# Kernel tuning notes

Measured on AMD Instinct MI355X. Metric: run time of the kernel, lower is better.

The kernel has to match this reference:

```python
import jax, jax.numpy as jnp
import numpy as np

LOG2PI = float(np.log(2.0 * np.pi))


def setup_inputs() -> dict:
    key = jax.random.key(0)
    ks = jax.random.split(key, 5)
    B, T, XD, C = 128, 2050, 6, 64
    return {
        "x": jax.random.normal(ks[0], (B, T, XD), jnp.float32),
        "observation_means": jax.random.uniform(ks[1], (C, XD), dtype=jnp.float32),
        "observation_stddevs": jax.random.uniform(ks[2], (C, XD), dtype=jnp.float32),
        "log_A": jax.random.normal(ks[3], (C, C), jnp.float32),
        "log_pi": jax.random.normal(ks[4], (C,), jnp.float32),
    }


def _emission_logprob(x, means, stds):
    # Normal(means[:, :4], relu(stds[:, :4]) + 0.1).log_prob(x[:, :, :4]) summed over feat dim
    mu = means[:, :4]                       # (C,4)
    sigma = jax.nn.relu(stds[:, :4]) + 0.1  # (C,4)
    z = (x[:, :, None, :4] - mu) / sigma    # (B,T,C,4)
    return jnp.sum(-0.5 * z * z - jnp.log(sigma) - 0.5 * LOG2PI, axis=-1)  # (B,T,C)


def _forward_scalers(logp, log_A, log_pi):
    # scaled HMM forward pass; returns per-step log normalizers (T,B)
    a0 = logp[:, 0] + log_pi
    s0 = jax.nn.logsumexp(a0, axis=-1)
    a0n = a0 - s0[:, None]

    def step(a_prev, lp_t):
        a = lp_t + jax.nn.logsumexp(a_prev[:, :, None] + log_A[None], axis=1)
        s = jax.nn.logsumexp(a, axis=-1)
        return a - s[:, None], s

    _, s_rest = jax.lax.scan(step, a0n, jnp.swapaxes(logp[:, 1:], 0, 1))
    return jnp.concatenate([s0[None], s_rest], axis=0)  # (T,B)


def _viterbi(logp, log_A, log_pi):
    d0 = logp[:, 0] + log_pi  # (B,C)

    def step(d_prev, lp_t):
        scores = d_prev[:, :, None] + log_A[None]  # (B,C_prev,C_cur)
        psi_t = jnp.argmax(scores, axis=1)
        d = jnp.max(scores, axis=1) + lp_t
        return d, psi_t

    d_last, psi = jax.lax.scan(step, d0, jnp.swapaxes(logp[:, 1:], 0, 1))  # psi: (T-1,B,C)
    c_last = jnp.argmax(d_last, axis=-1)  # (B,)

    def back(c_next, psi_t):
        c_t = jnp.take_along_axis(psi_t, c_next[:, None], axis=1)[:, 0]
        return c_t, c_t

    _, cs = jax.lax.scan(back, c_last, psi, reverse=True)  # (T-1,B)
    c = jnp.concatenate([cs, c_last[None]], axis=0)  # (T,B)
    return jnp.swapaxes(c, 0, 1)  # (B,T)


def reference(x, observation_means, observation_stddevs, log_A, log_pi):
    logA = jax.nn.log_softmax(log_A, axis=1)
    logpi = jax.nn.log_softmax(log_pi, axis=0)
    logp = _emission_logprob(x, observation_means, observation_stddevs)  # (B,T,C)
    scalers = _forward_scalers(logp, logA, logpi)                         # (T,B)
    logp_x = jnp.sum(scalers, axis=0)                                     # (B,)
    c_est = _viterbi(logp, logA, logpi)                                   # (B,T) int
    return logp_x, c_est
```

## Files before the change

kernel.cpp:

```cpp
#include <hip/hip_runtime.h>

#define T_LEN 2050
#define B_SZ 128
#define NCHUNK 33
#define HL2PI 0.91893853320467274178f

__device__ __forceinline__ float waveMax(float v) {
#pragma unroll
    for (int off = 32; off >= 1; off >>= 1)
        v = fmaxf(v, __shfl_xor(v, off, 64));
    return v;
}
__device__ __forceinline__ float waveSum(float v) {
#pragma unroll
    for (int off = 32; off >= 1; off >>= 1)
        v += __shfl_xor(v, off, 64);
    return v;
}
__device__ __forceinline__ void waveArgmax(float& v, int& idx) {
#pragma unroll
    for (int off = 32; off >= 1; off >>= 1) {
        float ov = __shfl_xor(v, off, 64);
        int   oi = __shfl_xor(idx, off, 64);
        if (ov > v || (ov == v && oi < idx)) { v = ov; idx = oi; }
    }
}
__device__ __forceinline__ void cfence() { asm volatile("" ::: "memory"); }

__device__ __forceinline__ float rl(float v, int lane) {
    return __int_as_float(__builtin_amdgcn_readlane(__float_as_int(v), lane));
}

__device__ __forceinline__ float dppSumAll(float v) {
#define SSTEP(ctrl) { int t_ = __builtin_amdgcn_update_dpp(0, __float_as_int(v), ctrl, 0xf, 0xf, true); \
                      v = v + __int_as_float(t_); }
    SSTEP(0x111) SSTEP(0x112) SSTEP(0x114) SSTEP(0x118) SSTEP(0x142) SSTEP(0x143)
#undef SSTEP
    return __int_as_float(__builtin_amdgcn_readlane(__float_as_int(v), 63));
}
__device__ __forceinline__ float dppMaxAll(float v) {
#define MSTEP(ctrl) { int t_ = __builtin_amdgcn_update_dpp(__float_as_int(v), __float_as_int(v), ctrl, 0xf, 0xf, false); \
                      v = fmaxf(v, __int_as_float(t_)); }
    MSTEP(0x111) MSTEP(0x112) MSTEP(0x114) MSTEP(0x118) MSTEP(0x142) MSTEP(0x143)
#undef MSTEP
    return __int_as_float(__builtin_amdgcn_readlane(__float_as_int(v), 63));
}

extern "C" __global__ __launch_bounds__(64, 1)
void hmm_prep(const float* __restrict__ logA_in,
              const float* __restrict__ logpi_in,
              float* __restrict__ lAg,
              float* __restrict__ lpig)
{
    __shared__ float la[64 * 65];
    __shared__ float rowlse[64];
    const int j = threadIdx.x;
#pragma unroll
    for (int k = 0; k < 64; ++k)
        la[k * 65 + j] = logA_in[k * 64 + j];
    cfence();
    {
        float m = -1e30f;
#pragma unroll
        for (int k = 0; k < 64; ++k) m = fmaxf(m, la[j * 65 + k]);
        float s = 0.f;
#pragma unroll
        for (int k = 0; k < 64; ++k) s += expf(la[j * 65 + k] - m);
        rowlse[j] = m + logf(s);
    }
    cfence();
    {
        float v = logpi_in[j];
        float m = waveMax(v);
        float s = waveSum(expf(v - m));
        lpig[j] = v - (m + logf(s));
    }
    float4* o = (float4*)lAg;
#pragma unroll
    for (int k = 0; k < 16; ++k) {
        float4 v;
        v.x = la[(4 * k + 0) * 65 + j] - rowlse[4 * k + 0];
        v.y = la[(4 * k + 1) * 65 + j] - rowlse[4 * k + 1];
        v.z = la[(4 * k + 2) * 65 + j] - rowlse[4 * k + 2];
        v.w = la[(4 * k + 3) * 65 + j] - rowlse[4 * k + 3];
        o[j * 16 + k] = v;
    }
}

extern "C" __global__ __launch_bounds__(256)
void hmm_emis(const float* __restrict__ x,
              const float* __restrict__ means,
              const float* __restrict__ stds,
              float* __restrict__ buf,
              float* __restrict__ m_pre)
{
    const int wid = blockIdx.x * 4 + (threadIdx.x >> 6);
    const int j = threadIdx.x & 63;
    const int t = wid >> 7;
    const int b = wid & 127;

    const float* xt = x + ((size_t)b * T_LEN + t) * 6;
    float x0 = xt[0], x1 = xt[1], x2 = xt[2], x3 = xt[3];

    float mu0 = means[j * 6 + 0], mu1 = means[j * 6 + 1];
    float mu2 = means[j * 6 + 2], mu3 = means[j * 6 + 3];
    float sg0 = fmaxf(stds[j * 6 + 0], 0.f) + 0.1f;
    float sg1 = fmaxf(stds[j * 6 + 1], 0.f) + 0.1f;
    float sg2 = fmaxf(stds[j * 6 + 2], 0.f) + 0.1f;
    float sg3 = fmaxf(stds[j * 6 + 3], 0.f) + 0.1f;
    float ls0 = logf(sg0), ls1 = logf(sg1), ls2 = logf(sg2), ls3 = logf(sg3);

    float z0 = (x0 - mu0) / sg0, z1 = (x1 - mu1) / sg1;
    float z2 = (x2 - mu2) / sg2, z3 = (x3 - mu3) / sg3;
    float e0 = ((-0.5f * z0) * z0 - ls0) - HL2PI;
    float e1 = ((-0.5f * z1) * z1 - ls1) - HL2PI;
    float e2 = ((-0.5f * z2) * z2 - ls2) - HL2PI;
    float e3 = ((-0.5f * z3) * z3 - ls3) - HL2PI;
    float lp = ((e0 + e1) + e2) + e3;

    buf[((size_t)b * T_LEN + t) * 64 + j] = lp;
    float mm = waveMax(lp);
    if (j == 0) m_pre[(size_t)b * T_LEN + t] = mm;
}

#define FWD_REDUCE(SRC)                                                   \
    float q0 = 0.f, q1 = 0.f, q2 = 0.f, q3 = 0.f;                         \
    _Pragma("unroll")                                                     \
    for (int gq = 0; gq < 4; ++gq) {                                      \
        float s_[16];                                                     \
        _Pragma("unroll")                                                 \
        for (int m_ = 0; m_ < 16; ++m_) s_[m_] = rl((SRC), 16 * gq + m_); \
        __builtin_amdgcn_sched_barrier(0);                                \
        _Pragma("unroll")                                                 \
        for (int k2 = 0; k2 < 4; ++k2) {                                  \
            const int i_ = 16 * gq + 4 * k2;                              \
            q0 = fmaf(s_[4 * k2 + 0], Ac[i_ + 0], q0);                    \
            q1 = fmaf(s_[4 * k2 + 1], Ac[i_ + 1], q1);                    \
            q2 = fmaf(s_[4 * k2 + 2], Ac[i_ + 2], q2);                    \
            q3 = fmaf(s_[4 * k2 + 3], Ac[i_ + 3], q3);                    \
        }                                                                 \
    }

#define FSTEP(LI, RN) {                                                   \
    const int l_ = l + (LI);                                              \
    float mm_c = rl(mA, l_);                                              \
    float y0 = rl(xA0, l_), y1 = rl(xA1, l_);                             \
    float y2 = rl(xA2, l_), y3 = rl(xA3, l_);                             \
    float w0 = (y0 - mu0) * i0, w1 = (y1 - mu1) * i1;                     \
    float w2 = (y2 - mu2) * i2, w3 = (y3 - mu3) * i3;                     \
    float lp = cst - 0.5f * (w0 * w0 + w1 * w1 + w2 * w2 + w3 * w3);      \
    float e_c = __expf(lp - mm_c);                                        \
    FWD_REDUCE(u);                                                        \
    u = ((q0 + q1) + (q2 + q3)) * e_c;                                    \
    acc += (double)mm_c;                                                  \
    if (RN) {                                                             \
        float ss = dppSumAll(u);                                          \
        acc += (double)__logf(ss);                                        \
        u *= (1.0f / ss);                                                 \
    }                                                                     \
}

#define VIT_REDUCE(SRC)                                                   \
    float m0 = -3.4e38f, m1 = -3.4e38f, m2 = -3.4e38f, m3 = -3.4e38f;     \
    _Pragma("unroll")                                                     \
    for (int gq = 0; gq < 4; ++gq) {                                      \
        float s_[16];                                                     \
        _Pragma("unroll")                                                 \
        for (int m_ = 0; m_ < 16; ++m_) s_[m_] = rl((SRC), 16 * gq + m_); \
        __builtin_amdgcn_sched_barrier(0);                                \
        _Pragma("unroll")                                                 \
        for (int k2 = 0; k2 < 4; k2 += 2) {                               \
            const int ia = 16 * gq + 4 * k2;                              \
            const int ib = ia + 4;                                        \
            float a0_ = s_[4*k2+0] + lA[ia+0], b0_ = s_[4*k2+4] + lA[ib+0]; \
            float a1_ = s_[4*k2+1] + lA[ia+1], b1_ = s_[4*k2+5] + lA[ib+1]; \
            float a2_ = s_[4*k2+2] + lA[ia+2], b2_ = s_[4*k2+6] + lA[ib+2]; \
            float a3_ = s_[4*k2+3] + lA[ia+3], b3_ = s_[4*k2+7] + lA[ib+3]; \
            m0 = fmaxf(fmaxf(m0, a0_), b0_);                              \
            m1 = fmaxf(fmaxf(m1, a1_), b1_);                              \
            m2 = fmaxf(fmaxf(m2, a2_), b2_);                              \
            m3 = fmaxf(fmaxf(m3, a3_), b3_);                              \
        }                                                                 \
    }

extern "C" __global__ __launch_bounds__(64, 1)
void hmm_main(const float* __restrict__ x,
              const float* __restrict__ means,
              const float* __restrict__ stds,
              const float* __restrict__ lAg,
              const float* __restrict__ lpig,
              float* __restrict__ out,
              float* __restrict__ buf,
              const float* __restrict__ m_pre,
              int* __restrict__ c_last)
{
    const int j   = threadIdx.x;
    const int bid = blockIdx.x;
    const bool is_fwd = (bid < B_SZ);
    const int b = is_fwd ? bid : bid - B_SZ;

    float lpi = lpig[j];

    if (is_fwd) {
        const float* xb = x + (size_t)b * T_LEN * 6;
        const float* mp = m_pre + (size_t)b * T_LEN;

        float mu0 = means[j * 6 + 0], mu1 = means[j * 6 + 1];
        float mu2 = means[j * 6 + 2], mu3 = means[j * 6 + 3];
        float sg0 = fmaxf(stds[j * 6 + 0], 0.f) + 0.1f;
        float sg1 = fmaxf(stds[j * 6 + 1], 0.f) + 0.1f;
        float sg2 = fmaxf(stds[j * 6 + 2], 0.f) + 0.1f;
        float sg3 = fmaxf(stds[j * 6 + 3], 0.f) + 0.1f;
        float ls0 = logf(sg0), ls1 = logf(sg1), ls2 = logf(sg2), ls3 = logf(sg3);
        float i0 = 1.f / sg0, i1 = 1.f / sg1, i2 = 1.f / sg2, i3 = 1.f / sg3;
        float cst = -(ls0 + ls1 + ls2 + ls3) - 4.f * HL2PI;

        float Ac[64];
        {
            const float4* g = (const float4*)lAg;
#pragma unroll
            for (int k = 0; k < 16; ++k) {
                float4 v = g[j * 16 + k];
                Ac[4 * k + 0] = __expf(v.x); Ac[4 * k + 1] = __expf(v.y);
                Ac[4 * k + 2] = __expf(v.z); Ac[4 * k + 3] = __expf(v.w);
            }
        }

        float z0 = (xb[0] - mu0) * i0, z1 = (xb[1] - mu1) * i1;
        float z2 = (xb[2] - mu2) * i2, z3 = (xb[3] - mu3) * i3;
        float a0 = (cst - 0.5f * (z0 * z0 + z1 * z1 + z2 * z2 + z3 * z3)) + lpi;
        float m0a = dppMaxAll(a0);
        float u = __expf(a0 - m0a);
        float s0 = dppSumAll(u);
        double acc = (double)(m0a + __logf(s0));
        u *= (1.0f / s0);

        float xA0, xA1, xA2, xA3, mA;
        {
            const float* p = xb + (size_t)(1 + j) * 6;
            xA0 = p[0]; xA1 = p[1]; xA2 = p[2]; xA3 = p[3];
            mA = mp[1 + j];
        }
        float xB0 = 0.f, xB1 = 0.f, xB2 = 0.f, xB3 = 0.f, mB = 0.f;

#pragma unroll 1
        for (int c = 0; c < 32; ++c) {
            if (c < 31) {
                const int idx = 65 + 64 * c + j;
                const float* p = xb + (size_t)idx * 6;
                xB0 = p[0]; xB1 = p[1]; xB2 = p[2]; xB3 = p[3];
                mB = mp[idx];
            }
#pragma unroll 1
            for (int l = 0; l < 64; l += 4) {
                FSTEP(0, false) FSTEP(1, false) FSTEP(2, false) FSTEP(3, true)
            }
            xA0 = xB0; xA1 = xB1; xA2 = xB2; xA3 = xB3; mA = mB;
        }
        {
            const float* p = xb + (size_t)2049 * 6;
            float y0 = p[0], y1 = p[1], y2 = p[2], y3 = p[3];
            float mm_c = mp[2049];
            float w0 = (y0 - mu0) * i0, w1 = (y1 - mu1) * i1;
            float w2 = (y2 - mu2) * i2, w3 = (y3 - mu3) * i3;
            float lp = cst - 0.5f * (w0 * w0 + w1 * w1 + w2 * w2 + w3 * w3);
            float e_c = __expf(lp - mm_c);
            FWD_REDUCE(u);
            u = ((q0 + q1) + (q2 + q3)) * e_c;
            acc += (double)mm_c;
        }
        float sf = dppSumAll(u);
        acc += (double)__logf(sf);
        if (j == 0) out[b] = (float)acc;
    } else {
        float lA[64];
        {
            const float4* g = (const float4*)lAg;
#pragma unroll
            for (int k = 0; k < 16; ++k) {
                float4 v = g[j * 16 + k];
                lA[4 * k + 0] = v.x; lA[4 * k + 1] = v.y;
                lA[4 * k + 2] = v.z; lA[4 * k + 3] = v.w;
            }
        }
        float* bb = buf + (size_t)b * T_LEN * 64 + j;

        float dn = bb[0] + lpi;
        float l0 = bb[64], l1 = bb[128], l2 = bb[192], l3 = bb[256];
        bb[0] = dn;

#pragma unroll 1
        for (int t = 1; t <= T_LEN - 5; ++t) {
            float lp_c = l0; l0 = l1; l1 = l2; l2 = l3;
            l3 = bb[(size_t)(t + 4) * 64];
            VIT_REDUCE(dn);
            dn = fmaxf(fmaxf(m0, m1), fmaxf(m2, m3)) + lp_c;
            bb[(size_t)t * 64] = dn;
        }
#pragma unroll 1
        for (int t = T_LEN - 4; t < T_LEN; ++t) {
            float lp_c = l0; l0 = l1; l1 = l2; l2 = l3;
            VIT_REDUCE(dn);
            dn = fmaxf(fmaxf(m0, m1), fmaxf(m2, m3)) + lp_c;
            bb[(size_t)t * 64] = dn;
        }

        float vv = dn; int idx = j;
        waveArgmax(vv, idx);
        if (j == 0) c_last[b] = idx;
    }
}

extern "C" __global__ __launch_bounds__(256)
void hmm_psi(const float* __restrict__ buf,
             const float* __restrict__ lAg,
             unsigned char* __restrict__ psi)
{
    __shared__ __align__(16) float sd[4][64];
    const int warp = threadIdx.x >> 6;
    const int j = threadIdx.x & 63;
    const int wid = blockIdx.x * 4 + warp;

    float lA[64];
    {
        const float4* g = (const float4*)lAg;
#pragma unroll
        for (int k = 0; k < 16; ++k) {
            float4 v = g[j * 16 + k];
            lA[4 * k + 0] = v.x; lA[4 * k + 1] = v.y;
            lA[4 * k + 2] = v.z; lA[4 * k + 3] = v.w;
        }
    }
    const float4* dv = (const float4*)sd[warp];
    const int NP = 2049 * B_SZ;

    for (int p = wid; p < NP; p += 8192) {
        const int t = (p >> 7) + 1;
        const int b = p & 127;
        float dval = buf[((size_t)b * T_LEN + (t - 1)) * 64 + j];
        sd[warp][j] = dval;

        float bv0 = -3.4e38f, bv1 = -3.4e38f, bv2 = -3.4e38f, bv3 = -3.4e38f;
        int bi0 = 0, bi1 = 1, bi2 = 2, bi3 = 3;
#pragma unroll
        for (int k = 0; k < 16; ++k) {
            float4 dd = dv[k];
            float v0 = dd.x + lA[4 * k + 0];
            float v1 = dd.y + lA[4 * k + 1];
            float v2 = dd.z + lA[4 * k + 2];
            float v3 = dd.w + lA[4 * k + 3];
            if (v0 > bv0) { bv0 = v0; bi0 = 4 * k + 0; }
            if (v1 > bv1) { bv1 = v1; bi1 = 4 * k + 1; }
            if (v2 > bv2) { bv2 = v2; bi2 = 4 * k + 2; }
            if (v3 > bv3) { bv3 = v3; bi3 = 4 * k + 3; }
        }
        float best = bv0; int bidx = bi0;
        if (bv1 > best || (bv1 == best && bi1 < bidx)) { best = bv1; bidx = bi1; }
        if (bv2 > best || (bv2 == best && bi2 < bidx)) { best = bv2; bidx = bi2; }
        if (bv3 > best || (bv3 == best && bi3 < bidx)) { best = bv3; bidx = bi3; }

        psi[((size_t)t * B_SZ + b) * 64 + j] = (unsigned char)bidx;
    }
}

extern "C" __global__ __launch_bounds__(256)
void hmm_compose(const unsigned char* __restrict__ psi,
                 unsigned char* __restrict__ mt)
{
    const int w = blockIdx.x * 4 + (threadIdx.x >> 6);
    const int j = threadIdx.x & 63;
    const int g = w % NCHUNK;
    const int b = w / NCHUNK;
    const int e = (g < NCHUNK - 1) ? g * 64 + 64 : (T_LEN - 1);
    int M = j;
    for (int t = e; t >= g * 64 + 1; --t)
        M = psi[((size_t)t * B_SZ + b) * 64 + M];
    mt[((size_t)g * B_SZ + b) * 64 + j] = (unsigned char)M;
}

extern "C" __global__ __launch_bounds__(64, 1)
void hmm_fill(const unsigned char* __restrict__ psi,
              const unsigned char* __restrict__ mt,
              const int* __restrict__ c_last,
              float* __restrict__ out)
{
    __shared__ int sb[NCHUNK];
    const int b = blockIdx.x;
    const int g = threadIdx.x;
    const int cl = c_last[b];
    if (g == 0) {
        int cur = cl;
        for (int q = NCHUNK - 1; q >= 0; --q) {
            cur = mt[((size_t)q * B_SZ + b) * 64 + cur];
            sb[q] = cur;
        }
    }
    cfence();
    float* oc = out + B_SZ + (size_t)b * T_LEN;
    if (g == NCHUNK) {
        oc[T_LEN - 1] = (float)cl;
    } else if (g < NCHUNK) {
        const int e = (g < NCHUNK - 1) ? g * 64 + 64 : (T_LEN - 1);
        int s = (g < NCHUNK - 1) ? sb[g + 1] : cl;
        for (int t = e; t >= g * 64 + 1; --t) {
            s = psi[((size_t)t * B_SZ + b) * 64 + s];
            oc[t - 1] = (float)s;
        }
    }
}

extern "C" void kernel_launch(void* const* d_in, const int* in_sizes, int n_in,
                              void* d_out, int out_size, void* d_ws, size_t ws_size,
                              hipStream_t stream)
{
    const float* x      = (const float*)d_in[0];
    const float* means  = (const float*)d_in[1];
    const float* stds   = (const float*)d_in[2];
    const float* logA   = (const float*)d_in[3];
    const float* logpi  = (const float*)d_in[4];
    float* out = (float*)d_out;

    char* base = (char*)d_ws;
    float*         buf   = (float*)base;
    unsigned char* psi   = (unsigned char*)(base + 67174400);
    float*         m_pre = (float*)(base + 67174400);
    unsigned char* mt    = (unsigned char*)(base + 83968000);
    int*           cl    = (int*)(base + 84238336);
    float*         lAg   = (float*)(base + 84238848);
    float*         lpig  = (float*)(base + 84255232);

    hipLaunchKernelGGL(hmm_prep, dim3(1), dim3(64), 0, stream, logA, logpi, lAg, lpig);
    hipLaunchKernelGGL(hmm_emis, dim3((T_LEN * B_SZ) / 4), dim3(256), 0, stream,
                       x, means, stds, buf, m_pre);
    hipLaunchKernelGGL(hmm_main, dim3(2 * B_SZ), dim3(64), 0, stream,
                       x, means, stds, lAg, lpig, out, buf, m_pre, cl);
    hipLaunchKernelGGL(hmm_psi, dim3(2048), dim3(256), 0, stream, buf, lAg, psi);
    hipLaunchKernelGGL(hmm_compose, dim3((NCHUNK * B_SZ) / 4), dim3(256), 0, stream, psi, mt);
    hipLaunchKernelGGL(hmm_fill, dim3(B_SZ), dim3(64), 0, stream, psi, mt, cl, out);
}
```

Baseline: 1.033 ms.

## Broadcast recurrence state through LDS and use packed f32x2 FMA/add

The per-step 64-lane state vector was previously broadcast with cross-lane register reads. Now each lane writes its value to a 64-float shared buffer and all lanes read it back as sixteen 128-bit vector loads. The transition matrix is also stored as float2 pairs, so the forward FMA and Viterbi add can use packed two-wide instructions. The aim is to cut the instruction count and the scalar-register dependency stalls on the serial time recurrence. In exchange, every step now pays an LDS write-then-read round trip on the critical dependency chain.

```diff
diff --git a/kernel.cpp b/kernel.cpp
--- a/kernel.cpp
+++ b/kernel.cpp
@@ -4,6 +4,9 @@
 #define B_SZ 128
 #define NCHUNK 33
 #define HL2PI 0.91893853320467274178f
+
+typedef __attribute__((ext_vector_type(2))) float f32x2;
+typedef __attribute__((ext_vector_type(4))) float f32x4;
 
 __device__ __forceinline__ float waveMax(float v) {
 #pragma unroll
@@ -123,21 +126,18 @@
     if (j == 0) m_pre[(size_t)b * T_LEN + t] = mm;
 }
 
-#define FWD_REDUCE(SRC)                                                   \
-    float q0 = 0.f, q1 = 0.f, q2 = 0.f, q3 = 0.f;                         \
-    _Pragma("unroll")                                                     \
-    for (int gq = 0; gq < 4; ++gq) {                                      \
-        float s_[16];                                                     \
+#define FWD_REDUCE_PK()                                                   \
+    f32x2 q01 = {0.f, 0.f}, q23 = {0.f, 0.f};                             \
+    {                                                                     \
+        f32x4 rr[16];                                                     \
         _Pragma("unroll")                                                 \
-        for (int m_ = 0; m_ < 16; ++m_) s_[m_] = rl((SRC), 16 * gq + m_); \
-        __builtin_amdgcn_sched_barrier(0);                                \
+        for (int k = 0; k < 16; ++k) rr[k] = pv[k];                       \
         _Pragma("unroll")                                                 \
-        for (int k2 = 0; k2 < 4; ++k2) {                                  \
-            const int i_ = 16 * gq + 4 * k2;                              \
-            q0 = fmaf(s_[4 * k2 + 0], Ac[i_ + 0], q0);                    \
-            q1 = fmaf(s_[4 * k2 + 1], Ac[i_ + 1], q1);                    \
-            q2 = fmaf(s_[4 * k2 + 2], Ac[i_ + 2], q2);                    \
-            q3 = fmaf(s_[4 * k2 + 3], Ac[i_ + 3], q3);                    \
+        for (int k = 0; k < 16; ++k) {                                    \
+            f32x2 s01 = __builtin_shufflevector(rr[k], rr[k], 0, 1);      \
+            f32x2 s23 = __builtin_shufflevector(rr[k], rr[k], 2, 3);      \
+            q01 = __builtin_elementwise_fma(s01, Ac2[2 * k + 0], q01);    \
+            q23 = __builtin_elementwise_fma(s23, Ac2[2 * k + 1], q23);    \
         }                                                                 \
     }
 
@@ -150,36 +150,34 @@
     float w2 = (y2 - mu2) * i2, w3 = (y3 - mu3) * i3;                     \
     float lp = cst - 0.5f * (w0 * w0 + w1 * w1 + w2 * w2 + w3 * w3);      \
     float e_c = __expf(lp - mm_c);                                        \
-    FWD_REDUCE(u);                                                        \
-    u = ((q0 + q1) + (q2 + q3)) * e_c;                                    \
+    FWD_REDUCE_PK();                                                      \
+    u = ((q01.x + q01.y) + (q23.x + q23.y)) * e_c;                        \
     acc += (double)mm_c;                                                  \
     if (RN) {                                                             \
         float ss = dppSumAll(u);                                          \
         acc += (double)__logf(ss);                                        \
         u *= (1.0f / ss);                                                 \
     }                                                                     \
-}
-
-#define VIT_REDUCE(SRC)                                                   \
+    pbuf[j] = u;                                                          \
+}
+
+#define VIT_REDUCE_PK()                                                   \
     float m0 = -3.4e38f, m1 = -3.4e38f, m2 = -3.4e38f, m3 = -3.4e38f;     \
-    _Pragma("unroll")                                                     \
-    for (int gq = 0; gq < 4; ++gq) {                                      \
-        float s_[16];                                                     \
+    {                                                                     \
+        f32x4 rr[16];                                                     \
         _Pragma("unroll")                                                 \
-        for (int m_ = 0; m_ < 16; ++m_) s_[m_] = rl((SRC), 16 * gq + m_); \
-        __builtin_amdgcn_sched_barrier(0);                                \
+        for (int k = 0; k < 16; ++k) rr[k] = pv[k];                       \
         _Pragma("unroll")                                                 \
-        for (int k2 = 0; k2 < 4; k2 += 2) {                               \
-            const int ia = 16 * gq + 4 * k2;                              \
-            const int ib = ia + 4;                                        \
-            float a0_ = s_[4*k2+0] + lA[ia+0], b0_ = s_[4*k2+4] + lA[ib+0]; \
-            float a1_ = s_[4*k2+1] + lA[ia+1], b1_ = s_[4*k2+5] + lA[ib+1]; \
-            float a2_ = s_[4*k2+2] + lA[ia+2], b2_ = s_[4*k2+6] + lA[ib+2]; \
-            float a3_ = s_[4*k2+3] + lA[ia+3], b3_ = s_[4*k2+7] + lA[ib+3]; \
-            m0 = fmaxf(fmaxf(m0, a0_), b0_);                              \
-            m1 = fmaxf(fmaxf(m1, a1_), b1_);                              \
-            m2 = fmaxf(fmaxf(m2, a2_), b2_);                              \
-            m3 = fmaxf(fmaxf(m3, a3_), b3_);                              \
+        for (int k2 = 0; k2 < 8; ++k2) {                                  \
+            f32x4 ra = rr[2 * k2], rb = rr[2 * k2 + 1];                   \
+            f32x2 va01 = __builtin_shufflevector(ra, ra, 0, 1) + lA2[4 * k2 + 0]; \
+            f32x2 va23 = __builtin_shufflevector(ra, ra, 2, 3) + lA2[4 * k2 + 1]; \
+            f32x2 vb01 = __builtin_shufflevector(rb, rb, 0, 1) + lA2[4 * k2 + 2]; \
+            f32x2 vb23 = __builtin_shufflevector(rb, rb, 2, 3) + lA2[4 * k2 + 3]; \
+            m0 = fmaxf(fmaxf(m0, va01.x), vb01.x);                        \
+            m1 = fmaxf(fmaxf(m1, va01.y), vb01.y);                        \
+            m2 = fmaxf(fmaxf(m2, va23.x), vb23.x);                        \
+            m3 = fmaxf(fmaxf(m3, va23.y), vb23.y);                        \
         }                                                                 \
     }
 
@@ -194,12 +192,15 @@
               const float* __restrict__ m_pre,
               int* __restrict__ c_last)
 {
+    __shared__ __align__(16) float pbuf[64];
+
     const int j   = threadIdx.x;
     const int bid = blockIdx.x;
     const bool is_fwd = (bid < B_SZ);
     const int b = is_fwd ? bid : bid - B_SZ;
 
     float lpi = lpig[j];
+    const f32x4* pv = (const f32x4*)pbuf;
 
     if (is_fwd) {
         const float* xb = x + (size_t)b * T_LEN * 6;
@@ -215,14 +216,14 @@
         float i0 = 1.f / sg0, i1 = 1.f / sg1, i2 = 1.f / sg2, i3 = 1.f / sg3;
         float cst = -(ls0 + ls1 + ls2 + ls3) - 4.f * HL2PI;
 
-        float Ac[64];
+        f32x2 Ac2[32];
         {
             const float4* g = (const float4*)lAg;
 #pragma unroll
             for (int k = 0; k < 16; ++k) {
                 float4 v = g[j * 16 + k];
-                Ac[4 * k + 0] = __expf(v.x); Ac[4 * k + 1] = __expf(v.y);
-                Ac[4 * k + 2] = __expf(v.z); Ac[4 * k + 3] = __expf(v.w);
+                Ac2[2 * k + 0] = f32x2{__expf(v.x), __expf(v.y)};
+                Ac2[2 * k + 1] = f32x2{__expf(v.z), __expf(v.w)};
             }
         }
 
@@ -234,6 +235,7 @@
         float s0 = dppSumAll(u);
         double acc = (double)(m0a + __logf(s0));
         u *= (1.0f / s0);
+        pbuf[j] = u;
 
         float xA0, xA1, xA2, xA3, mA;
         {
@@ -265,22 +267,22 @@
             float w2 = (y2 - mu2) * i2, w3 = (y3 - mu3) * i3;
             float lp = cst - 0.5f * (w0 * w0 + w1 * w1 + w2 * w2 + w3 * w3);
             float e_c = __expf(lp - mm_c);
-            FWD_REDUCE(u);
-            u = ((q0 + q1) + (q2 + q3)) * e_c;
+            FWD_REDUCE_PK();
+            u = ((q01.x + q01.y) + (q23.x + q23.y)) * e_c;
             acc += (double)mm_c;
         }
         float sf = dppSumAll(u);
         acc += (double)__logf(sf);
         if (j == 0) out[b] = (float)acc;
     } else {
-        float lA[64];
+        f32x2 lA2[32];
         {
             const float4* g = (const float4*)lAg;
 #pragma unroll
             for (int k = 0; k < 16; ++k) {
                 float4 v = g[j * 16 + k];
-                lA[4 * k + 0] = v.x; lA[4 * k + 1] = v.y;
-                lA[4 * k + 2] = v.z; lA[4 * k + 3] = v.w;
+                lA2[2 * k + 0] = f32x2{v.x, v.y};
+                lA2[2 * k + 1] = f32x2{v.z, v.w};
             }
         }
         float* bb = buf + (size_t)b * T_LEN * 64 + j;
@@ -288,21 +290,24 @@
         float dn = bb[0] + lpi;
         float l0 = bb[64], l1 = bb[128], l2 = bb[192], l3 = bb[256];
         bb[0] = dn;
+        pbuf[j] = dn;
 
 #pragma unroll 1
         for (int t = 1; t <= T_LEN - 5; ++t) {
             float lp_c = l0; l0 = l1; l1 = l2; l2 = l3;
             l3 = bb[(size_t)(t + 4) * 64];
-            VIT_REDUCE(dn);
+            VIT_REDUCE_PK();
             dn = fmaxf(fmaxf(m0, m1), fmaxf(m2, m3)) + lp_c;
             bb[(size_t)t * 64] = dn;
+            pbuf[j] = dn;
         }
 #pragma unroll 1
         for (int t = T_LEN - 4; t < T_LEN; ++t) {
             float lp_c = l0; l0 = l1; l1 = l2; l2 = l3;
-            VIT_REDUCE(dn);
+            VIT_REDUCE_PK();
             dn = fmaxf(fmaxf(m0, m1), fmaxf(m2, m3)) + lp_c;
             bb[(size_t)t * 64] = dn;
+            pbuf[j] = dn;
         }
 
         float vv = dn; int idx = j;
```

Measured after the change: 1.064 ms. 2.9% more time.
